# Optimization experiments

Measured on AMD Instinct MI355X. Metric: run time of the kernel, lower is better.

Reference implementation:

```python
import jax, jax.numpy as jnp
import numpy as np

H = 2048            # hidden_size
HK, HV = 16, 32     # num_k_heads, num_v_heads
DK, DV = 128, 128   # head dims
KEY_DIM = HK * DK   # 2048
VAL_DIM = HV * DV   # 4096
CONV_DIM = 2 * KEY_DIM + VAL_DIM  # 8192
KW = 4              # conv kernel width
CS = 64             # chunk size
B, S = 2, 4096
EPS = 1e-6


def setup_inputs() -> dict:
    key = jax.random.key(0)
    ks = jax.random.split(key, 8)
    sc = lambda n: 1.0 / np.sqrt(n)
    return {
        "hidden_states": jax.random.normal(ks[0], (B, S, H), jnp.float32),
        "W_qkvz": jax.random.normal(ks[1], (H, 2 * KEY_DIM + 2 * VAL_DIM), jnp.float32) * sc(H),
        "W_ba": jax.random.normal(ks[2], (H, 2 * HV), jnp.float32) * sc(H),
        "conv_w": jax.random.normal(ks[3], (CONV_DIM, KW), jnp.float32) * sc(KW),
        "A_log": jnp.log(jax.random.uniform(ks[4], (HV,), jnp.float32, 1.0, 16.0)),
        "dt_bias": jax.random.normal(ks[5], (HV,), jnp.float32) * 0.1,
        "norm_weight": jnp.ones((DV,), jnp.float32),
        "W_out": jax.random.normal(ks[6], (VAL_DIM, H), jnp.float32) * sc(VAL_DIM),
    }


def l2norm(x, eps=1e-6):
    return x * jax.lax.rsqrt(jnp.sum(x * x, -1, keepdims=True) + eps)


def chunk_gated_delta_rule(q, k, v, g, beta):
    # q,k: (B,S,HV,DK); v: (B,S,HV,DV); g,beta: (B,S,HV). S divisible by CS.
    q = l2norm(q)
    k = l2norm(k)
    tr = lambda x: jnp.swapaxes(x, 1, 2).astype(jnp.float32)  # -> (B,H,S,...)
    q, k, v = tr(q), tr(k), tr(v)
    g = jnp.swapaxes(g, 1, 2).astype(jnp.float32)
    beta = jnp.swapaxes(beta, 1, 2).astype(jnp.float32)
    q = q * (1.0 / np.sqrt(DK))
    nc = S // CS
    rs = lambda x: x.reshape(B, HV, nc, CS, x.shape[-1])
    v_beta = v * beta[..., None]
    k_beta = k * beta[..., None]
    q, k, v, k_beta, v_beta = map(rs, (q, k, v, k_beta, v_beta))
    g = jnp.cumsum(g.reshape(B, HV, nc, CS), -1)
    tril = jnp.tril(jnp.ones((CS, CS), bool))
    diff = g[..., :, None] - g[..., None, :]
    decay = jnp.exp(jnp.where(tril, diff, 0.0)) * tril  # (B,H,nc,CS,CS)
    # strictly-lower A; the original sequential loop computes T = (I - A)^{-1}
    A = -jnp.tril(jnp.einsum('bhcid,bhcjd->bhcij', k_beta, k) * decay, -1)
    eye = jnp.eye(CS, dtype=jnp.float32)
    T = jax.scipy.linalg.solve_triangular(
        eye - A, jnp.broadcast_to(eye, A.shape), lower=True, unit_diagonal=True)
    v_t = jnp.einsum('bhcij,bhcjd->bhcid', T, v_beta)
    k_cumdecay = jnp.einsum('bhcij,bhcjd->bhcid', T, k_beta * jnp.exp(g)[..., None])
    strict_low = jnp.tril(jnp.ones((CS, CS), jnp.float32), -1)

    def step(state, xs):
        q_i, k_i, v_i, kc_i, g_i, dm_i = xs  # (B,H,CS,*)
        attn = jnp.einsum('bhid,bhjd->bhij', q_i, k_i) * dm_i * strict_low
        v_new = v_i - kc_i @ state
        out = (q_i * jnp.exp(g_i)[..., None]) @ state + attn @ v_new
        g_last = g_i[..., -1]
        state = state * jnp.exp(g_last)[..., None, None] + jnp.einsum(
            'bhcd,bhcv->bhdv', k_i * jnp.exp(g_last[..., None] - g_i)[..., None], v_new)
        return state, out

    S0 = jnp.zeros((B, HV, DK, DV), jnp.float32)
    mv = lambda x: jnp.moveaxis(x, 2, 0)  # chunk axis first for scan
    _, outs = jax.lax.scan(step, S0, (mv(q), mv(k), mv(v_t), mv(k_cumdecay), mv(g), mv(decay)))
    out = jnp.moveaxis(outs, 0, 2).reshape(B, HV, S, DV)
    return jnp.swapaxes(out, 1, 2)  # (B,S,HV,DV)


def reference(hidden_states, W_qkvz, W_ba, conv_w, A_log, dt_bias, norm_weight, W_out):
    r = HV // HK
    qkvz = hidden_states @ W_qkvz                     # (B,S,2*KEY+2*VAL)
    ba = hidden_states @ W_ba                         # (B,S,2*HV)
    qkvz = qkvz.reshape(B, S, HK, 2 * DK + 2 * r * DV)
    q, k, v, z = jnp.split(qkvz, [DK, 2 * DK, 2 * DK + r * DV], axis=-1)
    v = v.reshape(B, S, HV, DV)
    z = z.reshape(B, S, HV, DV)
    ba = ba.reshape(B, S, HK, 2 * r)
    b, a = jnp.split(ba, [r], axis=-1)
    b = b.reshape(B, S, HV)
    a = a.reshape(B, S, HV)
    # fused causal depthwise conv + silu over [q|k|v]
    mixed = jnp.concatenate([q.reshape(B, S, -1), k.reshape(B, S, -1), v.reshape(B, S, -1)], -1)
    x = jnp.swapaxes(mixed, 1, 2)                     # (B, CONV_DIM, S)
    xp = jnp.pad(x, ((0, 0), (0, 0), (KW - 1, 0)))
    conv = sum(conv_w[:, j][None, :, None] * xp[:, :, j:j + S] for j in range(KW))
    conv = jax.nn.silu(conv)
    qkv = jnp.swapaxes(conv, 1, 2)
    q, k, v = jnp.split(qkv, [KEY_DIM, 2 * KEY_DIM], axis=-1)
    q = q.reshape(B, S, HK, DK)
    k = k.reshape(B, S, HK, DK)
    v = v.reshape(B, S, HV, DV)
    beta = jax.nn.sigmoid(b)
    g = -jnp.exp(A_log) * jax.nn.softplus(a + dt_bias)
    q = jnp.repeat(q, r, axis=2)
    k = jnp.repeat(k, r, axis=2)
    core = chunk_gated_delta_rule(q, k, v, g, beta)   # (B,S,HV,DV)
    # gated RMSNorm over head_v_dim
    cf = core.astype(jnp.float32)
    var = jnp.mean(cf * cf, -1, keepdims=True)
    core = cf * jax.lax.rsqrt(var + EPS) * norm_weight
    core = core * jax.nn.silu(z.astype(jnp.float32))
    return core.reshape(B, S, VAL_DIM) @ W_out        # (B,S,H)
```

## Files before the change

### kernel.cpp

```cpp
#include <hip/hip_runtime.h>
#include <cstdint>
#include <cstddef>


typedef _Float16 half_t;
typedef _Float16 half2_t __attribute__((ext_vector_type(2)));
typedef _Float16 half4_t __attribute__((ext_vector_type(4)));
typedef _Float16 half8   __attribute__((ext_vector_type(8)));
typedef float    f32x4   __attribute__((ext_vector_type(4)));

#define MFMA16(a, b, c) __builtin_amdgcn_mfma_f32_16x16x32_f16((a), (b), (c), 0, 0, 0)

#define AS1 __attribute__((address_space(1)))
#define AS3 __attribute__((address_space(3)))

__device__ __forceinline__ void gload16(void* lds, const void* g) {
    __builtin_amdgcn_global_load_lds((AS1 void*)(g), (AS3 void*)(lds), 16, 0, 0);
}

__device__ __forceinline__ void at_wr(float* AT, int i, int j, float v) {
    *(float*)((char*)AT + i * 256 + ((j * 4) ^ ((i & 7) << 4))) = v;
}
__device__ __forceinline__ half8 frag64(const half_t* base, int row, int koff) {
    return *(const half8*)((const char*)base + row * 128 + ((koff * 2) ^ ((row & 7) << 4)));
}
__device__ __forceinline__ void w64(half_t* base, int row, int col, float v) {
    *(half_t*)((char*)base + row * 128 + ((col * 2) ^ ((row & 7) << 4))) = (half_t)v;
}
__device__ __forceinline__ half8 frag128(const half_t* base, int row, int koff) {
    return *(const half8*)((const char*)base + row * 256 + ((koff * 2) ^ ((row & 7) << 4)));
}

__global__ __launch_bounds__(256) void prep_k(const float* __restrict__ hidden,
                                              const float* __restrict__ Wq,
                                              const float* __restrict__ Wba,
                                              const float* __restrict__ Wo,
                                              half_t* __restrict__ hiddenH,
                                              half_t* __restrict__ W1T,
                                              half_t* __restrict__ WoT) {
    __shared__ half_t tile[32][33];
    const int bid = blockIdx.x;
    if (bid < 2048) {
        const long n4 = (long)8192 * 2048 / 4;
        for (long i = (long)bid * 256 + threadIdx.x; i < n4; i += (long)2048 * 256) {
            f32x4 v = *(const f32x4*)(hidden + i * 4);
            half4_t h;
            h[0] = (half_t)v[0]; h[1] = (half_t)v[1];
            h[2] = (half_t)v[2]; h[3] = (half_t)v[3];
            *(half4_t*)(hiddenH + i * 4) = h;
        }
        return;
    }
    int tx = threadIdx.x & 31, ty = threadIdx.x >> 5;
    if (bid < 27136) {
        int idx = bid - 2048;
        int n0 = (idx % 392) * 32, k0 = (idx / 392) * 32;
#pragma unroll
        for (int t = 0; t < 4; ++t) {
            int k = k0 + ty + t * 8, n = n0 + tx;
            float v = 0.f;
            if (n < 2048) {
                int kh = n >> 7, d = n & 127;
                v = Wq[(long)k * 12288 + kh * 768 + d];
            } else if (n < 4096) {
                int n2 = n - 2048; int kh = n2 >> 7, d = n2 & 127;
                v = Wq[(long)k * 12288 + kh * 768 + 128 + d];
            } else if (n < 8192) {
                int n3 = n - 4096; int vh = n3 >> 7, d = n3 & 127;
                int kh = vh >> 1, jj = vh & 1;
                v = Wq[(long)k * 12288 + kh * 768 + 256 + jj * 128 + d];
            } else if (n < 8256) {
                v = Wba[(long)k * 64 + (n - 8192)];
            } else if (n >= 8448) {
                int n4 = n - 8448; int vh = n4 >> 7, d = n4 & 127;
                int kh = vh >> 1, jj = vh & 1;
                v = Wq[(long)k * 12288 + kh * 768 + 512 + jj * 128 + d];
            }
            tile[ty + t * 8][tx] = (half_t)v;
        }
        __syncthreads();
#pragma unroll
        for (int t = 0; t < 4; ++t) {
            int n = n0 + ty + t * 8, k = k0 + tx;
            W1T[(long)n * 2048 + k] = tile[tx][ty + t * 8];
        }
        return;
    }
    {
        int idx = bid - 27136;
        int n0 = (idx % 64) * 32, k0 = (idx / 64) * 32;
#pragma unroll
        for (int t = 0; t < 4; ++t) {
            int k = k0 + ty + t * 8, n = n0 + tx;
            tile[ty + t * 8][tx] = (half_t)Wo[(long)k * 2048 + n];
        }
        __syncthreads();
#pragma unroll
        for (int t = 0; t < 4; ++t) {
            int n = n0 + ty + t * 8, k = k0 + tx;
            WoT[(long)n * 4096 + k] = tile[tx][ty + t * 8];
        }
    }
}

template <int OUT_F16>
__global__ __launch_bounds__(1024, 4) void gemm256_k(const half_t* __restrict__ A,
                                                     const half_t* __restrict__ Bt,
                                                     void* __restrict__ C,
                                                     void* __restrict__ C2,
                                                     int K, int ldc, int ldc2,
                                                     int nwgM, int nwgN, int tnSplit) {
    __shared__ half_t LA[2][2][8192];
    __shared__ half_t LB[2][2][8192];
    const int tid = threadIdx.x, lane = tid & 63, w = tid >> 6;
    const int lo = lane & 15, hi = lane >> 4;
    const int wm = w >> 2, wn = w & 3;
    const int nwg = gridDim.x, q = nwg >> 3, bid = blockIdx.x;
    const int swz = (bid & 7) * q + (bid >> 3);
    const int grp = 8 * nwgN;
    const int gid = swz / grp;
    const int rem = swz - gid * grp;
    const int fm = gid * 8;
    const int gsz = min(nwgM - fm, 8);
    const long tm = fm + rem % gsz;
    const long tn = rem / gsz;
    const long Kb = (long)K * 2;
    const char* Ab = (const char*)A + tm * 256 * Kb;
    const char* Bb = (const char*)Bt + tn * 256 * Kb;
    void* Cp;
    long ld, col0;
    if ((int)tn < tnSplit) { Cp = C;  ld = ldc;  col0 = tn * 256; }
    else                   { Cp = C2; ld = ldc2; col0 = (tn - tnSplit) * 256; }
    const int scol = ((lane & 7) << 4) ^ ((lane >> 3) << 4);
    const int srow = lane >> 3;
    const int sa0 = w * 2, sa1 = w * 2 + 1;

    auto stSeg = [&](half_t (*L)[2][8192], const char* gb0, int kt, int s) {
        int h = s >> 4, si = s & 15;
        gload16((char*)&L[kt & 1][h][0] + si * 1024,
                gb0 + (long)(h * 128 + si * 8 + srow) * Kb + (long)kt * 128 + scol);
    };
    auto stTile = [&](int kt) {
        stSeg(LA, Ab, kt, sa0); stSeg(LA, Ab, kt, sa1);
        stSeg(LB, Bb, kt, sa0); stSeg(LB, Bb, kt, sa1);
    };
    auto rdA = [&](int p, int mt, int kc) -> half8 {
        int r = wm * 64 + mt * 16 + lo;
        int rl = r & 127;
        return *(const half8*)((const char*)&LA[p][r >> 7][0] + rl * 128 +
                               ((kc * 64 + hi * 16) ^ ((rl & 7) << 4)));
    };
    auto rdB = [&](int p, int nt, int kc) -> half8 {
        int r = wn * 64 + nt * 16 + lo;
        int rl = r & 127;
        return *(const half8*)((const char*)&LB[p][r >> 7][0] + rl * 128 +
                               ((kc * 64 + hi * 16) ^ ((rl & 7) << 4)));
    };

    f32x4 acc[4][4] = {};
    half8 af[4], bf[4];

    auto rdFrags = [&](int p, int kc) {
#pragma unroll
        for (int mt = 0; mt < 4; ++mt) af[mt] = rdA(p, mt, kc);
#pragma unroll
        for (int nt = 0; nt < 4; ++nt) bf[nt] = rdB(p, nt, kc);
    };
    auto mfmaQ = [&]() {
#pragma unroll
        for (int mt = 0; mt < 4; ++mt)
#pragma unroll
            for (int nt = 0; nt < 4; ++nt)
                acc[mt][nt] = MFMA16(af[mt], bf[nt], acc[mt][nt]);
    };

    const int nkt = K >> 6;
    stTile(0); stTile(1);
    asm volatile("s_waitcnt vmcnt(4)" ::: "memory");
    __builtin_amdgcn_s_barrier();

    for (int kt = 0; kt < nkt; ++kt) {
        const int p = kt & 1;
        rdFrags(p, 0);
        mfmaQ();
        rdFrags(p, 1);
        asm volatile("s_waitcnt lgkmcnt(0)" ::: "memory");
        __builtin_amdgcn_s_barrier();
        if (kt + 2 < nkt) {
            stTile(kt + 2);
            asm volatile("s_waitcnt vmcnt(4)" ::: "memory");
        } else if (kt + 1 < nkt) {
            asm volatile("s_waitcnt vmcnt(0)" ::: "memory");
        }
        __builtin_amdgcn_s_barrier();
        mfmaQ();
    }

    const long crow0 = tm * 256 + wm * 64 + hi * 4;
    const long ccol0 = col0 + wn * 64 + lo;
#pragma unroll
    for (int mt = 0; mt < 4; ++mt)
#pragma unroll
        for (int nt = 0; nt < 4; ++nt)
#pragma unroll
            for (int e = 0; e < 4; ++e) {
                long row = crow0 + mt * 16 + e;
                long col = ccol0 + nt * 16;
                if (OUT_F16)
                    ((half_t*)Cp)[row * ld + col] = (half_t)acc[mt][nt][e];
                else
                    ((float*)Cp)[row * ld + col] = acc[mt][nt][e];
            }
}

__global__ __launch_bounds__(256) void conv_silu_k(const half_t* __restrict__ mixedH,
                                                   const float* __restrict__ conv_w,
                                                   half_t* __restrict__ qb,
                                                   half_t* __restrict__ kb,
                                                   half_t* __restrict__ vb) {
    const int ldm = 8448;
    int bx = blockIdx.x;
    int ch0 = (bx * 256 + threadIdx.x) * 8;
    int b = blockIdx.y >> 7, sc = blockIdx.y & 127;
    int s0 = sc * 32;
    half_t* dptr;
    long dstr;
    float nsc = 1.f;
    bool donorm = (bx < 2);
    if (bx == 0)      { dptr = qb + ch0;          dstr = 2048; nsc = 0.08838834764831845f; }
    else if (bx == 1) { dptr = kb + (ch0 - 2048); dstr = 2048; }
    else              { dptr = vb + (ch0 - 4096); dstr = 4096; }
    float w0[8], w1[8], w2[8], w3[8];
#pragma unroll
    for (int j = 0; j < 8; ++j) {
        f32x4 wv = *(const f32x4*)(conv_w + (ch0 + j) * 4);
        w0[j] = wv[0]; w1[j] = wv[1]; w2[j] = wv[2]; w3[j] = wv[3];
    }
    const half_t* src = mixedH + (long)b * 4096 * ldm + ch0;
    half8 x0 = {}, x1 = {}, x2 = {};
    if (s0 >= 3) {
        x0 = *(const half8*)(src + (long)(s0 - 3) * ldm);
        x1 = *(const half8*)(src + (long)(s0 - 2) * ldm);
        x2 = *(const half8*)(src + (long)(s0 - 1) * ldm);
    }
    for (int s = s0; s < s0 + 32; ++s) {
        half8 x3 = *(const half8*)(src + (long)s * ldm);
        float y[8];
        float ss = 0.f;
#pragma unroll
        for (int j = 0; j < 8; ++j) {
            float t = w0[j] * (float)x0[j] + w1[j] * (float)x1[j] +
                      w2[j] * (float)x2[j] + w3[j] * (float)x3[j];
            t = t / (1.f + __expf(-t));
            y[j] = t;
            ss += t * t;
        }
        half8 yv;
        if (donorm) {
            ss += __shfl_xor(ss, 1);
            ss += __shfl_xor(ss, 2);
            ss += __shfl_xor(ss, 4);
            ss += __shfl_xor(ss, 8);
            float r = rsqrtf(ss + 1e-6f) * nsc;
#pragma unroll
            for (int j = 0; j < 8; ++j) yv[j] = (half_t)(y[j] * r);
        } else {
#pragma unroll
            for (int j = 0; j < 8; ++j) yv[j] = (half_t)y[j];
        }
        *(half8*)(dptr + ((long)b * 4096 + s) * dstr) = yv;
        x0 = x1; x1 = x2; x2 = x3;
    }
}

__global__ __launch_bounds__(256) void gate_beta_k(const half_t* __restrict__ mixedH,
                                                   const float* __restrict__ A_log,
                                                   const float* __restrict__ dt_bias,
                                                   float* __restrict__ beta,
                                                   float* __restrict__ gcum) {
    __shared__ float gs[32][64];
    int b = blockIdx.x >> 6, c = blockIdx.x & 63;
    for (int idx = threadIdx.x; idx < 2048; idx += 256) {
        int vh = idx & 31, i = idx >> 5;
        int kh = vh >> 1, j = vh & 1;
        long row = ((long)b * 4096 + c * 64 + i) * 8448 + 8192 + kh * 4;
        float bb = (float)mixedH[row + j];
        float aa = (float)mixedH[row + 2 + j];
        beta[((long)b * 4096 + c * 64 + i) * 32 + vh] = 1.f / (1.f + __expf(-bb));
        float x = aa + dt_bias[vh];
        float sp = (x > 15.f) ? x : log1pf(__expf(x));
        gs[vh][i] = -__expf(A_log[vh]) * sp;
    }
    __syncthreads();
    if (threadIdx.x < 32) {
        int vh = threadIdx.x;
        float cum = 0.f;
        float* gout = gcum + ((long)(b * 32 + vh)) * 4096 + c * 64;
        for (int i = 0; i < 64; ++i) { cum += gs[vh][i]; gout[i] = cum; }
    }
}

__global__ __launch_bounds__(256) void phase1_k(const half_t* __restrict__ qb,
                                                const half_t* __restrict__ kb,
                                                const half_t* __restrict__ vb,
                                                const float* __restrict__ beta,
                                                const float* __restrict__ gcum,
                                                half_t* __restrict__ attnW,
                                                half_t* __restrict__ vtW,
                                                half_t* __restrict__ kcW) {
    __shared__ float AT[64 * 64];
    __shared__ half_t XT[256 * 64];
    __shared__ float gcS[64], betaS[64], egS[64];
    int blk = blockIdx.x;
    int c = blk & 63, vh = (blk >> 6) & 31, b = blk >> 11;
    int kh = vh >> 1;
    int tid = threadIdx.x, lane = tid & 63, w = tid >> 6, lo = lane & 15, hi = lane >> 4;
    long rowbase = (long)b * 4096 + c * 64;
    if (tid < 64) {
        float g = gcum[((long)(b * 32 + vh)) * 4096 + c * 64 + tid];
        gcS[tid] = g; egS[tid] = __expf(g);
        betaS[tid] = beta[(rowbase + tid) * 32 + vh];
    }
    const half_t* kR = kb + rowbase * 2048 + kh * 128;
    const half_t* qR = qb + rowbase * 2048 + kh * 128;
    f32x4 accG[4] = {}, accA[4] = {};
#pragma unroll
    for (int kt = 0; kt < 4; ++kt) {
        half8 ak = *(const half8*)(kR + (long)(w * 16 + lo) * 2048 + kt * 32 + hi * 8);
        half8 aq = *(const half8*)(qR + (long)(w * 16 + lo) * 2048 + kt * 32 + hi * 8);
#pragma unroll
        for (int n = 0; n < 4; ++n) {
            half8 bk = *(const half8*)(kR + (long)(n * 16 + lo) * 2048 + kt * 32 + hi * 8);
            accG[n] = MFMA16(ak, bk, accG[n]);
            accA[n] = MFMA16(aq, bk, accA[n]);
        }
    }
    __syncthreads();
    half_t* attnB = attnW + (long)blk * 4096;
#pragma unroll
    for (int n = 0; n < 4; ++n)
#pragma unroll
        for (int e = 0; e < 4; ++e) {
            int i = w * 16 + hi * 4 + e;
            int j = n * 16 + lo;
            float dec = (j < i) ? __expf(gcS[i] - gcS[j]) : 0.f;
            float av = (j < i) ? (-betaS[i] * accG[n][e] * dec) : (j == i ? 1.f : 0.f);
            at_wr(AT, i, j, av);
            attnB[(long)i * 64 + j] = (half_t)((j < i) ? accA[n][e] * dec : 0.f);
        }
    __syncthreads();
    if (w == 0) {
        float t[64];
#pragma unroll
        for (int i = 0; i < 64; ++i) t[i] = (lane == i) ? 1.f : 0.f;
#pragma unroll
        for (int i = 1; i < 64; ++i) {
            float a0 = 0.f, a1 = 0.f, a2 = 0.f, a3 = 0.f;
#pragma unroll
            for (int p0 = 0; p0 < i; p0 += 4) {
                f32x4 a4 = *(const f32x4*)((const char*)AT + i * 256 +
                                           ((p0 * 4) ^ ((i & 7) << 4)));
                if (p0 + 0 < i) a0 += a4[0] * t[p0 + 0];
                if (p0 + 1 < i) a1 += a4[1] * t[p0 + 1];
                if (p0 + 2 < i) a2 += a4[2] * t[p0 + 2];
                if (p0 + 3 < i) a3 += a4[3] * t[p0 + 3];
            }
            t[i] += (a0 + a1) + (a2 + a3);
        }
        half_t* TS = (half_t*)AT;
#pragma unroll
        for (int i = 0; i < 64; ++i)
            *(half_t*)((char*)TS + i * 128 + ((lane * 2) ^ ((i & 7) << 4))) = (half_t)t[i];
    } else {
        for (int idx = tid - 64; idx < 4096; idx += 192) {
            int p = idx >> 6, dp = idx & 63;
            float bb = betaS[p], be = betaS[p] * egS[p];
            half2_t vv = *(const half2_t*)(vb + (rowbase + p) * 4096 + vh * 128 + dp * 2);
            half2_t kk = *(const half2_t*)(kb + (rowbase + p) * 2048 + kh * 128 + dp * 2);
            w64(XT, dp * 2,       p, (float)vv[0] * bb);
            w64(XT, dp * 2 + 1,   p, (float)vv[1] * bb);
            w64(XT, 128 + dp * 2,     p, (float)kk[0] * be);
            w64(XT, 128 + dp * 2 + 1, p, (float)kk[1] * be);
        }
    }
    __syncthreads();
    const half_t* TS = (const half_t*)AT;
    f32x4 accO[4][4] = {};
#pragma unroll
    for (int kt = 0; kt < 2; ++kt) {
        half8 tf[4];
#pragma unroll
        for (int m = 0; m < 4; ++m) tf[m] = frag64(TS, m * 16 + lo, kt * 32 + hi * 8);
#pragma unroll
        for (int n = 0; n < 4; ++n) {
            half8 bx = frag64(XT, w * 64 + n * 16 + lo, kt * 32 + hi * 8);
#pragma unroll
            for (int m = 0; m < 4; ++m) accO[m][n] = MFMA16(tf[m], bx, accO[m][n]);
        }
    }
    long ob = (long)blk * 8192;
#pragma unroll
    for (int m = 0; m < 4; ++m)
#pragma unroll
        for (int n = 0; n < 4; ++n)
#pragma unroll
            for (int e = 0; e < 4; ++e) {
                int i = m * 16 + hi * 4 + e;
                int dc = w * 64 + n * 16 + lo;
                float v = accO[m][n][e];
                if (dc < 128) vtW[ob + (long)i * 128 + dc] = (half_t)v;
                else          kcW[ob + (long)i * 128 + dc - 128] = (half_t)(-v);
            }
}

struct P2Ops {
    half8 kcf[4], qf[4], k8[4];
    half8 atf[2];
    half_t vtv[8];
    float gm, gi, g63;
};

__global__ __launch_bounds__(256, 1) void phase2_k(const half_t* __restrict__ qb,
                                                   const half_t* __restrict__ kb,
                                                   const float* __restrict__ gcum,
                                                   const half_t* __restrict__ attnW,
                                                   const half_t* __restrict__ vtW,
                                                   const half_t* __restrict__ kcW,
                                                   half_t* __restrict__ coreH) {
    __shared__ half_t SHs[32 * 128];
    __shared__ half_t vnT[32 * 64];
    __shared__ half_t kdT[128 * 64];
    int blk = blockIdx.x;
    int bvh = blk & 63, js = blk >> 6;
    int vh = bvh & 31, b = bvh >> 5, kh = vh >> 1;
    int j0 = js * 32;
    int tid = threadIdx.x, lane = tid & 63, w = tid >> 6, lo = lane & 15, hi = lane >> 4;
    int ii = tid >> 2, dseg = tid & 3;
    int jm = w >> 1, dql = (w & 1) * 4;
    for (int idx = tid; idx < 32 * 128; idx += 256) SHs[idx] = (half_t)0.f;
    __syncthreads();
    const float* gbase = gcum + (long)bvh * 4096;

    auto loadops = [&](int c, P2Ops& o) {
        long pb = (long)bvh * 64 + c;
        const half_t* kcG = kcW + pb * 8192;
        const half_t* vtG = vtW + pb * 8192;
        const half_t* atG = attnW + pb * 4096;
        long rowbase = (long)b * 4096 + c * 64;
        const float* gp = gbase + c * 64;
#pragma unroll
        for (int kt = 0; kt < 4; ++kt) {
            o.kcf[kt] = *(const half8*)(kcG + (long)(w * 16 + lo) * 128 + kt * 32 + hi * 8);
            o.qf[kt] = *(const half8*)(qb + (rowbase + w * 16 + lo) * 2048 + kh * 128 +
                                       kt * 32 + hi * 8);
        }
#pragma unroll
        for (int kt2 = 0; kt2 < 2; ++kt2)
            o.atf[kt2] = *(const half8*)(atG + (long)(w * 16 + lo) * 64 + kt2 * 32 + hi * 8);
#pragma unroll
        for (int s = 0; s < 4; ++s)
            o.k8[s] = *(const half8*)(kb + (rowbase + ii) * 2048 + kh * 128 + dseg * 32 + s * 8);
#pragma unroll
        for (int n = 0; n < 2; ++n)
#pragma unroll
            for (int e = 0; e < 4; ++e)
                o.vtv[n * 4 + e] = vtG[(long)(w * 16 + hi * 4 + e) * 128 + j0 + n * 16 + lo];
        o.gm = gp[w * 16 + lo];
        o.gi = gp[ii];
        o.g63 = gp[63];
    };

    auto step = [&](int c, P2Ops& o, P2Ops& nx) {
        long rowbase = (long)b * 4096 + c * 64;
        loadops(c + 1 < 64 ? c + 1 : 63, nx);
        half8 bS[4][2];
#pragma unroll
        for (int kt = 0; kt < 4; ++kt) {
            bS[kt][0] = frag128(SHs, lo, kt * 32 + hi * 8);
            bS[kt][1] = frag128(SHs, 16 + lo, kt * 32 + hi * 8);
        }
        f32x4 accV[2];
#pragma unroll
        for (int n = 0; n < 2; ++n)
#pragma unroll
            for (int e = 0; e < 4; ++e) accV[n][e] = (float)o.vtv[n * 4 + e];
#pragma unroll
        for (int kt = 0; kt < 4; ++kt) {
            accV[0] = MFMA16(o.kcf[kt], bS[kt][0], accV[0]);
            accV[1] = MFMA16(o.kcf[kt], bS[kt][1], accV[1]);
        }
#pragma unroll
        for (int n = 0; n < 2; ++n) {
            int j = n * 16 + lo, i0 = w * 16 + hi * 4;
            half4_t h4;
            h4[0] = (half_t)accV[n][0]; h4[1] = (half_t)accV[n][1];
            h4[2] = (half_t)accV[n][2]; h4[3] = (half_t)accV[n][3];
            *(half4_t*)((char*)vnT + j * 128 + ((i0 * 2) ^ ((j & 7) << 4))) = h4;
        }
        {
            float ek = __expf(o.g63 - o.gi);
#pragma unroll
            for (int s = 0; s < 4; ++s)
#pragma unroll
                for (int e2 = 0; e2 < 8; ++e2)
                    w64(kdT, dseg * 32 + s * 8 + e2, ii, (float)o.k8[s][e2] * ek);
        }
        __syncthreads();
        float egm = __expf(o.gm);
        f32x4 accO[2] = {};
#pragma unroll
        for (int kt = 0; kt < 4; ++kt) {
            half8 aq;
#pragma unroll
            for (int e2 = 0; e2 < 8; ++e2) aq[e2] = (half_t)((float)o.qf[kt][e2] * egm);
            accO[0] = MFMA16(aq, bS[kt][0], accO[0]);
            accO[1] = MFMA16(aq, bS[kt][1], accO[1]);
        }
#pragma unroll
        for (int kt2 = 0; kt2 < 2; ++kt2) {
            half8 bV0 = frag64(vnT, lo, kt2 * 32 + hi * 8);
            half8 bV1 = frag64(vnT, 16 + lo, kt2 * 32 + hi * 8);
            accO[0] = MFMA16(o.atf[kt2], bV0, accO[0]);
            accO[1] = MFMA16(o.atf[kt2], bV1, accO[1]);
        }
        f32x4 accU[4] = {};
#pragma unroll
        for (int kt2 = 0; kt2 < 2; ++kt2) {
            half8 avn = frag64(vnT, jm * 16 + lo, kt2 * 32 + hi * 8);
#pragma unroll
            for (int dnn = 0; dnn < 4; ++dnn) {
                half8 bkd = frag64(kdT, (dql + dnn) * 16 + lo, kt2 * 32 + hi * 8);
                accU[dnn] = MFMA16(avn, bkd, accU[dnn]);
            }
        }
#pragma unroll
        for (int n = 0; n < 2; ++n)
#pragma unroll
            for (int e = 0; e < 4; ++e)
                coreH[(rowbase + w * 16 + hi * 4 + e) * 4096 + vh * 128 + j0 + n * 16 + lo] =
                    (half_t)accO[n][e];
        __syncthreads();
        float egl = __expf(o.g63);
#pragma unroll
        for (int dnn = 0; dnn < 4; ++dnn)
#pragma unroll
            for (int e = 0; e < 4; ++e) {
                int j = jm * 16 + hi * 4 + e;
                int d = (dql + dnn) * 16 + lo;
                char* p = (char*)SHs + j * 256 + ((d * 2) ^ ((j & 7) << 4));
                float old = (float)*(half_t*)p;
                *(half_t*)p = (half_t)(old * egl + accU[dnn][e]);
            }
        __syncthreads();
    };

    P2Ops opsA, opsB;
    loadops(0, opsA);
    for (int c = 0; c < 64; c += 2) {
        step(c, opsA, opsB);
        step(c + 1, opsB, opsA);
    }
}

__global__ __launch_bounds__(256) void normgate_k(half_t* __restrict__ coreH,
                                                  const half_t* __restrict__ zH,
                                                  const float* __restrict__ norm_w) {
    int w = threadIdx.x >> 6, lane = threadIdx.x & 63;
    float w0 = norm_w[lane * 2], w1 = norm_w[lane * 2 + 1];
    for (long rid = (long)blockIdx.x * 4 + w; rid < 262144; rid += (long)gridDim.x * 4) {
        long bs = rid >> 5;
        int vh = rid & 31;
        half_t* cr = coreH + bs * 4096 + vh * 128;
        half2_t cv = *(half2_t*)(cr + lane * 2);
        float f0 = (float)cv[0], f1 = (float)cv[1];
        float ss = f0 * f0 + f1 * f1;
#pragma unroll
        for (int off = 32; off; off >>= 1) ss += __shfl_xor(ss, off);
        float rs = rsqrtf(ss * (1.f / 128.f) + 1e-6f);
        half2_t zz = *(const half2_t*)(zH + bs * 4096 + vh * 128 + lane * 2);
        float z0 = (float)zz[0], z1 = (float)zz[1];
        float s0 = z0 / (1.f + __expf(-z0)), s1 = z1 / (1.f + __expf(-z1));
        half2_t o;
        o[0] = (half_t)(f0 * rs * w0 * s0);
        o[1] = (half_t)(f1 * rs * w1 * s1);
        *(half2_t*)(cr + lane * 2) = o;
    }
}

extern "C" void kernel_launch(void* const* d_in, const int* in_sizes, int n_in,
                              void* d_out, int out_size, void* d_ws, size_t ws_size,
                              hipStream_t stream) {
    const float* hidden  = (const float*)d_in[0];
    const float* W_qkvz  = (const float*)d_in[1];
    const float* W_ba    = (const float*)d_in[2];
    const float* conv_w  = (const float*)d_in[3];
    const float* A_log   = (const float*)d_in[4];
    const float* dt_bias = (const float*)d_in[5];
    const float* norm_w  = (const float*)d_in[6];
    const float* W_out   = (const float*)d_in[7];
    float* out = (float*)d_out;

    char* ws = (char*)d_ws;
    const size_t MB = 1ull << 20;
    half_t* qb      = (half_t*)(ws + 0);
    half_t* kb      = (half_t*)(ws + 32 * MB);
    half_t* vb      = (half_t*)(ws + 64 * MB);
    float*  betaB   = (float*) (ws + 128 * MB);
    float*  gcum    = (float*) (ws + 129 * MB);
    half_t* WoT     = (half_t*)(ws + 130 * MB);
    half_t* zH      = (half_t*)(ws + 146 * MB);
    half_t* mixedH  = (half_t*)(ws + 210 * MB);
    half_t* attnW   = (half_t*)(ws + 210 * MB);
    half_t* vtW     = (half_t*)(ws + 242 * MB);
    half_t* kcW     = (half_t*)(ws + 306 * MB);
    half_t* hiddenH = (half_t*)(ws + 0);
    half_t* W1T     = (half_t*)(ws + 32 * MB);
    half_t* coreH   = (half_t*)(ws + 64 * MB);
    (void)ws_size; (void)in_sizes; (void)n_in; (void)out_size;

    prep_k<<<35328, 256, 0, stream>>>(hidden, W_qkvz, W_ba, W_out,
                                      hiddenH, W1T, WoT);
    gemm256_k<1><<<1568, 1024, 0, stream>>>(hiddenH, W1T, mixedH, zH,
                                            2048, 8448, 4096, 32, 49, 33);
    conv_silu_k<<<dim3(4, 256), 256, 0, stream>>>(mixedH, conv_w, qb, kb, vb);
    gate_beta_k<<<128, 256, 0, stream>>>(mixedH, A_log, dt_bias, betaB, gcum);
    phase1_k<<<4096, 256, 0, stream>>>(qb, kb, vb, betaB, gcum, attnW, vtW, kcW);
    phase2_k<<<256, 256, 0, stream>>>(qb, kb, gcum, attnW, vtW, kcW, coreH);
    normgate_k<<<4096, 256, 0, stream>>>(coreH, zH, norm_w);
    gemm256_k<0><<<256, 1024, 0, stream>>>(coreH, WoT, out, nullptr,
                                           4096, 2048, 0, 32, 8, 8);
}
```

Measured before the change: 1.062 ms.

## Split phase2 state columns into 16-wide slices to double block count

The sequential chunk-recurrence kernel now gives each block 16 value columns of the state instead of 32, so it launches 512 blocks instead of 256 and asks for two blocks per CU. This aims to fill more of the GPU's compute units during the serial 64-chunk loop. In exchange, each block redundantly reloads and recomputes the shared per-chunk operands (the kcW, q, k and attention fragments and the kdT staging), roughly doubling that traffic and work.

```diff
diff --git a/kernel.cpp b/kernel.cpp
--- a/kernel.cpp
+++ b/kernel.cpp
@@ -416,28 +416,27 @@
 struct P2Ops {
     half8 kcf[4], qf[4], k8[4];
     half8 atf[2];
-    half_t vtv[8];
+    half_t vtv[4];
     float gm, gi, g63;
 };
 
-__global__ __launch_bounds__(256, 1) void phase2_k(const half_t* __restrict__ qb,
+__global__ __launch_bounds__(256, 2) void phase2_k(const half_t* __restrict__ qb,
                                                    const half_t* __restrict__ kb,
                                                    const float* __restrict__ gcum,
                                                    const half_t* __restrict__ attnW,
                                                    const half_t* __restrict__ vtW,
                                                    const half_t* __restrict__ kcW,
                                                    half_t* __restrict__ coreH) {
-    __shared__ half_t SHs[32 * 128];
-    __shared__ half_t vnT[32 * 64];
+    __shared__ half_t SHs[16 * 128];
+    __shared__ half_t vnT[16 * 64];
     __shared__ half_t kdT[128 * 64];
     int blk = blockIdx.x;
     int bvh = blk & 63, js = blk >> 6;
     int vh = bvh & 31, b = bvh >> 5, kh = vh >> 1;
-    int j0 = js * 32;
+    int j0 = js * 16;
     int tid = threadIdx.x, lane = tid & 63, w = tid >> 6, lo = lane & 15, hi = lane >> 4;
     int ii = tid >> 2, dseg = tid & 3;
-    int jm = w >> 1, dql = (w & 1) * 4;
-    for (int idx = tid; idx < 32 * 128; idx += 256) SHs[idx] = (half_t)0.f;
+    for (int idx = tid; idx < 16 * 128; idx += 256) SHs[idx] = (half_t)0.f;
     __syncthreads();
     const float* gbase = gcum + (long)bvh * 4096;
 
@@ -461,10 +460,8 @@
         for (int s = 0; s < 4; ++s)
             o.k8[s] = *(const half8*)(kb + (rowbase + ii) * 2048 + kh * 128 + dseg * 32 + s * 8);
 #pragma unroll
-        for (int n = 0; n < 2; ++n)
-#pragma unroll
-            for (int e = 0; e < 4; ++e)
-                o.vtv[n * 4 + e] = vtG[(long)(w * 16 + hi * 4 + e) * 128 + j0 + n * 16 + lo];
+        for (int e = 0; e < 4; ++e)
+            o.vtv[e] = vtG[(long)(w * 16 + hi * 4 + e) * 128 + j0 + lo];
         o.gm = gp[w * 16 + lo];
         o.gi = gp[ii];
         o.g63 = gp[63];
@@ -473,28 +470,19 @@
     auto step = [&](int c, P2Ops& o, P2Ops& nx) {
         long rowbase = (long)b * 4096 + c * 64;
         loadops(c + 1 < 64 ? c + 1 : 63, nx);
-        half8 bS[4][2];
-#pragma unroll
-        for (int kt = 0; kt < 4; ++kt) {
-            bS[kt][0] = frag128(SHs, lo, kt * 32 + hi * 8);
-            bS[kt][1] = frag128(SHs, 16 + lo, kt * 32 + hi * 8);
-        }
-        f32x4 accV[2];
-#pragma unroll
-        for (int n = 0; n < 2; ++n)
-#pragma unroll
-            for (int e = 0; e < 4; ++e) accV[n][e] = (float)o.vtv[n * 4 + e];
-#pragma unroll
-        for (int kt = 0; kt < 4; ++kt) {
-            accV[0] = MFMA16(o.kcf[kt], bS[kt][0], accV[0]);
-            accV[1] = MFMA16(o.kcf[kt], bS[kt][1], accV[1]);
-        }
-#pragma unroll
-        for (int n = 0; n < 2; ++n) {
-            int j = n * 16 + lo, i0 = w * 16 + hi * 4;
+        half8 bS[4];
+#pragma unroll
+        for (int kt = 0; kt < 4; ++kt) bS[kt] = frag128(SHs, lo, kt * 32 + hi * 8);
+        f32x4 accV;
+#pragma unroll
+        for (int e = 0; e < 4; ++e) accV[e] = (float)o.vtv[e];
+#pragma unroll
+        for (int kt = 0; kt < 4; ++kt) accV = MFMA16(o.kcf[kt], bS[kt], accV);
+        {
+            int j = lo, i0 = w * 16 + hi * 4;
             half4_t h4;
-            h4[0] = (half_t)accV[n][0]; h4[1] = (half_t)accV[n][1];
-            h4[2] = (half_t)accV[n][2]; h4[3] = (half_t)accV[n][3];
+            h4[0] = (half_t)accV[0]; h4[1] = (half_t)accV[1];
+            h4[2] = (half_t)accV[2]; h4[3] = (half_t)accV[3];
             *(half4_t*)((char*)vnT + j * 128 + ((i0 * 2) ^ ((j & 7) << 4))) = h4;
         }
         {
@@ -507,49 +495,44 @@
         }
         __syncthreads();
         float egm = __expf(o.gm);
-        f32x4 accO[2] = {};
+        f32x4 accO = {};
 #pragma unroll
         for (int kt = 0; kt < 4; ++kt) {
             half8 aq;
 #pragma unroll
             for (int e2 = 0; e2 < 8; ++e2) aq[e2] = (half_t)((float)o.qf[kt][e2] * egm);
-            accO[0] = MFMA16(aq, bS[kt][0], accO[0]);
-            accO[1] = MFMA16(aq, bS[kt][1], accO[1]);
-        }
+            accO = MFMA16(aq, bS[kt], accO);
+        }
+        half8 avn[2];
 #pragma unroll
         for (int kt2 = 0; kt2 < 2; ++kt2) {
-            half8 bV0 = frag64(vnT, lo, kt2 * 32 + hi * 8);
-            half8 bV1 = frag64(vnT, 16 + lo, kt2 * 32 + hi * 8);
-            accO[0] = MFMA16(o.atf[kt2], bV0, accO[0]);
-            accO[1] = MFMA16(o.atf[kt2], bV1, accO[1]);
-        }
-        f32x4 accU[4] = {};
+            avn[kt2] = frag64(vnT, lo, kt2 * 32 + hi * 8);
+            accO = MFMA16(o.atf[kt2], avn[kt2], accO);
+        }
+        f32x4 accU[2] = {};
 #pragma unroll
         for (int kt2 = 0; kt2 < 2; ++kt2) {
-            half8 avn = frag64(vnT, jm * 16 + lo, kt2 * 32 + hi * 8);
-#pragma unroll
-            for (int dnn = 0; dnn < 4; ++dnn) {
-                half8 bkd = frag64(kdT, (dql + dnn) * 16 + lo, kt2 * 32 + hi * 8);
-                accU[dnn] = MFMA16(avn, bkd, accU[dnn]);
+#pragma unroll
+            for (int t = 0; t < 2; ++t) {
+                half8 bkd = frag64(kdT, (2 * w + t) * 16 + lo, kt2 * 32 + hi * 8);
+                accU[t] = MFMA16(avn[kt2], bkd, accU[t]);
             }
         }
 #pragma unroll
-        for (int n = 0; n < 2; ++n)
-#pragma unroll
-            for (int e = 0; e < 4; ++e)
-                coreH[(rowbase + w * 16 + hi * 4 + e) * 4096 + vh * 128 + j0 + n * 16 + lo] =
-                    (half_t)accO[n][e];
+        for (int e = 0; e < 4; ++e)
+            coreH[(rowbase + w * 16 + hi * 4 + e) * 4096 + vh * 128 + j0 + lo] =
+                (half_t)accO[e];
         __syncthreads();
         float egl = __expf(o.g63);
 #pragma unroll
-        for (int dnn = 0; dnn < 4; ++dnn)
+        for (int t = 0; t < 2; ++t)
 #pragma unroll
             for (int e = 0; e < 4; ++e) {
-                int j = jm * 16 + hi * 4 + e;
-                int d = (dql + dnn) * 16 + lo;
+                int j = hi * 4 + e;
+                int d = (2 * w + t) * 16 + lo;
                 char* p = (char*)SHs + j * 256 + ((d * 2) ^ ((j & 7) << 4));
                 float old = (float)*(half_t*)p;
-                *(half_t*)p = (half_t)(old * egl + accU[dnn][e]);
+                *(half_t*)p = (half_t)(old * egl + accU[t][e]);
             }
         __syncthreads();
     };
@@ -625,7 +608,7 @@
     conv_silu_k<<<dim3(4, 256), 256, 0, stream>>>(mixedH, conv_w, qb, kb, vb);
     gate_beta_k<<<128, 256, 0, stream>>>(mixedH, A_log, dt_bias, betaB, gcum);
     phase1_k<<<4096, 256, 0, stream>>>(qb, kb, vb, betaB, gcum, attnW, vtW, kcW);
-    phase2_k<<<256, 256, 0, stream>>>(qb, kb, gcum, attnW, vtW, kcW, coreH);
+    phase2_k<<<512, 256, 0, stream>>>(qb, kb, gcum, attnW, vtW, kcW, coreH);
     normgate_k<<<4096, 256, 0, stream>>>(coreH, zH, norm_w);
     gemm256_k<0><<<256, 1024, 0, stream>>>(coreH, WoT, out, nullptr,
                                            4096, 2048, 0, 32, 8, 8);
```

New measurement: 1.139 ms. +7.2%, slower.
